# Kernel optimization log

Measured on AMD Instinct MI355X. Metric: run time of the kernel, lower is better.

The kernel has to match this reference:

```python
import jax, jax.numpy as jnp
import numpy as np

NODES = 163842
IN_FEATS = 32
OUT_FEATS = 64

def setup_inputs() -> dict:
    key = jax.random.key(0)
    k1, k2, k3, k4, k5 = jax.random.split(key, 5)
    x = jax.random.normal(k1, (NODES, IN_FEATS), dtype=jnp.float32)
    # 0-based neighbor indices (original stores 1-based and subtracts 1)
    neigh_indices = jax.random.randint(k2, (NODES, 25, 3), 0, NODES, dtype=jnp.int32)
    # barycentric interpolation weights per (node, 25 template positions, 3 triangle verts)
    neigh_weights = jax.random.uniform(k3, (NODES, 25, 3), dtype=jnp.float32)
    W = jax.random.normal(k4, (OUT_FEATS, 25 * IN_FEATS), dtype=jnp.float32) * 0.02
    b = jax.random.normal(k5, (OUT_FEATS,), dtype=jnp.float32) * 0.02
    return {"x": x, "neigh_indices": neigh_indices, "neigh_weights": neigh_weights, "W": W, "b": b}

def reference(x, neigh_indices, neigh_weights, W, b):
    nodes, c = x.shape
    # gather neighbor features: (nodes, 25, 3, in_feats)
    mat = x[neigh_indices.reshape(-1)].reshape(nodes, 25, 3, c)
    # barycentric weighted sum over the 3 triangle vertices -> (nodes, 25, in_feats)
    feat = jnp.sum(mat * neigh_weights[..., None], axis=2)
    # flatten the 25 template positions and project: (nodes, out_feats)
    feat = feat.reshape(nodes, 25 * c)
    return feat @ W.T + b
```

## Files before the change

### kernel.cpp

```cpp
#include <hip/hip_runtime.h>
#include <hip/hip_bf16.h>
#include <type_traits>

#define NNODES   163842
#define INF      32
#define OUTF     64
#define NPOS     25
#define KTOT     800
#define MT       64
#define NTHREADS 256

typedef float    f32x4 __attribute__((ext_vector_type(4)));
typedef _Float16 f16x8 __attribute__((ext_vector_type(8)));

__global__ void cvt_kernel(const float* __restrict__ x, const float* __restrict__ W,
                           _Float16* __restrict__ xh, _Float16* __restrict__ wh) {
    int tid = blockIdx.x * blockDim.x + threadIdx.x;
    int stride = gridDim.x * blockDim.x;
    const int nx8 = NNODES * INF / 8;
    const f32x4* x4 = (const f32x4*)x;
    f16x8* xh8 = (f16x8*)xh;
    for (int j = tid; j < nx8; j += stride) {
        f32x4 a = x4[2*j], b = x4[2*j+1];
        f16x8 o;
        #pragma unroll
        for (int k = 0; k < 4; ++k) { o[k] = (_Float16)a[k]; o[4+k] = (_Float16)b[k]; }
        xh8[j] = o;
    }
    f16x8* wh8 = (f16x8*)wh;
    for (int t = tid; t < NPOS * 4 * 64; t += stride) {
        const int l  = t & 63;
        const int nb = (t >> 6) & 3;
        const int p  = t >> 8;
        const int row = 16*nb + (l & 15);
        const int kb  = p*32 + (l >> 4)*8;
        const float* src = W + row * KTOT + kb;
        f16x8 o;
        #pragma unroll
        for (int j = 0; j < 8; ++j) o[j] = (_Float16)src[j];
        wh8[t] = o;
    }
}

__launch_bounds__(NTHREADS, 2)
__global__ void conv_mfma(const int* __restrict__ nidx, const float* __restrict__ nwt,
                          const _Float16* __restrict__ xh, const _Float16* __restrict__ wh,
                          const float* __restrict__ bias, float* __restrict__ out) {
    __shared__ int      idxs[MT * 75];
    __shared__ _Float16 wtsl[MT * 76];

    const int tid = threadIdx.x;
    const int blk = blockIdx.x;

    {
        const long gbase = (long)blk * (MT * 75);
        const long tot   = (long)NNODES * 75;
        #pragma unroll
        for (int it = 0; it < (MT * 75 + NTHREADS - 1) / NTHREADS; ++it) {
            int i = tid + it * NTHREADS;
            if (i < MT * 75) {
                long g = gbase + i;
                bool ok = g < tot;
                int n = i / 75, t = i % 75;
                idxs[i] = ok ? nidx[g] : 0;
                wtsl[n * 76 + t] = ok ? (_Float16)nwt[g] : (_Float16)0.0f;
            }
        }
    }

    const int lane = tid & 63;
    const int wave = tid >> 6;
    const int arow = lane & 15;
    const int kgrp = lane >> 4;
    const int irow = (wave * 16 + arow) * 75;
    const int wrow = (wave * 16 + arow) * 76;
    const int node0 = blk * MT + wave * 16;
    const _Float16* xg = xh + kgrp * 8;

    __syncthreads();

    f32x4 acc[4] = {{0,0,0,0},{0,0,0,0},{0,0,0,0},{0,0,0,0}};
    f16x8 gA[9], gB[9];
    f16x8 bA[12], bB[12];

    #define SB() __builtin_amdgcn_sched_barrier(0)

    auto BLD = [&](f16x8* b, int g, auto CNT) {
        constexpr int C = decltype(CNT)::value;
        #pragma unroll
        for (int q = 0; q < 4 * C; ++q) {
            const int f = g * 12 + q;
            b[q] = *(const f16x8*)(wh + (long)f * 512 + lane * 8);
        }
    };
    auto GATH = [&](f16x8* v, int g, auto CNT) {
        constexpr int C = decltype(CNT)::value;
        #pragma unroll
        for (int t = 0; t < 3 * C; ++t) {
            const int idx = idxs[irow + g * 9 + t];
            v[t] = *(const f16x8*)(xg + (long)idx * INF);
        }
    };
    auto COMP = [&](const f16x8* v, const f16x8* b, int g, auto CNT) {
        constexpr int C = decltype(CNT)::value;
        #pragma unroll
        for (int p = 0; p < C; ++p) {
            const int pos = g * 3 + p;
            const _Float16 w0 = wtsl[wrow + pos*3 + 0];
            const _Float16 w1 = wtsl[wrow + pos*3 + 1];
            const _Float16 w2 = wtsl[wrow + pos*3 + 2];
            f16x8 af = v[p*3+0] * w0 + v[p*3+1] * w1 + v[p*3+2] * w2;
            #pragma unroll
            for (int nb = 0; nb < 4; ++nb)
                acc[nb] = __builtin_amdgcn_mfma_f32_16x16x32_f16(b[p*4+nb], af, acc[nb], 0, 0, 0);
        }
    };

    constexpr std::integral_constant<int,3> C3{};
    constexpr std::integral_constant<int,1> C1{};

    BLD(bA,0,C3); GATH(gA,0,C3); SB();
    BLD(bB,1,C3); GATH(gB,1,C3); SB();
    COMP(gA,bA,0,C3); SB(); BLD(bA,2,C3); GATH(gA,2,C3); SB();
    COMP(gB,bB,1,C3); SB(); BLD(bB,3,C3); GATH(gB,3,C3); SB();
    COMP(gA,bA,2,C3); SB(); BLD(bA,4,C3); GATH(gA,4,C3); SB();
    COMP(gB,bB,3,C3); SB(); BLD(bB,5,C3); GATH(gB,5,C3); SB();
    COMP(gA,bA,4,C3); SB(); BLD(bA,6,C3); GATH(gA,6,C3); SB();
    COMP(gB,bB,5,C3); SB(); BLD(bB,7,C3); GATH(gB,7,C3); SB();
    COMP(gA,bA,6,C3); SB(); BLD(bA,8,C1); GATH(gA,8,C1); SB();
    COMP(gB,bB,7,C3); SB();
    COMP(gA,bA,8,C1);

    const int node = node0 + arow;
    if (node < NNODES) {
        #pragma unroll
        for (int nb = 0; nb < 4; ++nb) {
            const int cb = 16*nb + 4*kgrp;
            const f32x4 b4 = *(const f32x4*)(bias + cb);
            f32x4 o;
            #pragma unroll
            for (int r = 0; r < 4; ++r) o[r] = acc[nb][r] + b4[r];
            *(f32x4*)(out + (long)node * OUTF + cb) = o;
        }
    }
    #undef SB
}

__global__ void conv_fallback(const float* __restrict__ x, const int* __restrict__ nidx,
                              const float* __restrict__ nwt, const float* __restrict__ W,
                              const float* __restrict__ bias, float* __restrict__ out) {
    __shared__ float feat[KTOT];
    const int n = blockIdx.x;
    const int t = threadIdx.x;
    for (int e = t; e < KTOT; e += 64) {
        const int p = e >> 5, c = e & 31;
        const int ib = n * 75 + p * 3;
        float a = 0.0f;
        #pragma unroll
        for (int v = 0; v < 3; ++v)
            a += nwt[ib+v] * x[nidx[ib+v] * INF + c];
        feat[e] = a;
    }
    __syncthreads();
    float a = bias[t];
    const float* wr = W + t * KTOT;
    for (int k = 0; k < KTOT; ++k) a += feat[k] * wr[k];
    out[(long)n * OUTF + t] = a;
}

extern "C" void kernel_launch(void* const* d_in, const int* in_sizes, int n_in,
                              void* d_out, int out_size, void* d_ws, size_t ws_size,
                              hipStream_t stream) {
    const float* x    = (const float*)d_in[0];
    const int*   nidx = (const int*)  d_in[1];
    const float* nwt  = (const float*)d_in[2];
    const float* W    = (const float*)d_in[3];
    const float* bias = (const float*)d_in[4];
    float* out = (float*)d_out;

    const size_t need = (size_t)NNODES * INF * 2 + (size_t)NPOS * 4 * 64 * 8 * 2;
    if (ws_size < need) {
        conv_fallback<<<NNODES, 64, 0, stream>>>(x, nidx, nwt, W, bias, out);
        return;
    }

    _Float16* xh = (_Float16*)d_ws;
    _Float16* wh = xh + (size_t)NNODES * INF;

    cvt_kernel<<<1024, NTHREADS, 0, stream>>>(x, W, xh, wh);
    const int nblocks = (NNODES + MT - 1) / MT;
    conv_mfma<<<nblocks, NTHREADS, 0, stream>>>(nidx, nwt, xh, wh, bias, out);
}
```

Measured before the change: 179.3 us.

## Gather neighbor features directly into LDS with a per-position 3-deep load pipeline

Replaces the register-based double-buffered gather of feature rows and weight fragments with global_load_lds direct-to-LDS loads for neighbor features, plus inline-asm weight loads into a 4-slot register ring. Each template position is processed as one step with an explicit vmcnt wait, keeping three positions of loads in flight. The aim is to cut VGPR pressure and raise occupancy and memory-level parallelism for the random gathers. In exchange it adds 48KB of LDS per block, which may limit blocks per CU, and relies on hand-counted vmcnt values that must match the number of issued loads.

```diff
diff --git a/kernel.cpp b/kernel.cpp
--- a/kernel.cpp
+++ b/kernel.cpp
@@ -12,6 +12,20 @@
 
 typedef float    f32x4 __attribute__((ext_vector_type(4)));
 typedef _Float16 f16x8 __attribute__((ext_vector_type(8)));
+
+template<int N> using IC = std::integral_constant<int, N>;
+
+typedef const __attribute__((address_space(1))) void GV;
+typedef __attribute__((address_space(3))) void LV;
+
+template<int N>
+__device__ __forceinline__ void waitv_sb() {
+    static_assert(N == 0 || N == 7 || N == 14, "bad vmcnt");
+    if constexpr (N == 14)      asm volatile("s_waitcnt vmcnt(14)" ::: "memory");
+    else if constexpr (N == 7)  asm volatile("s_waitcnt vmcnt(7)"  ::: "memory");
+    else                        asm volatile("s_waitcnt vmcnt(0)"  ::: "memory");
+    __builtin_amdgcn_sched_barrier(0);
+}
 
 __global__ void cvt_kernel(const float* __restrict__ x, const float* __restrict__ W,
                            _Float16* __restrict__ xh, _Float16* __restrict__ wh) {
@@ -48,6 +62,7 @@
                           const float* __restrict__ bias, float* __restrict__ out) {
     __shared__ int      idxs[MT * 75];
     __shared__ _Float16 wtsl[MT * 76];
+    __shared__ __align__(16) _Float16 feat[4][4][3][512];
 
     const int tid = threadIdx.x;
     const int blk = blockIdx.x;
@@ -75,61 +90,60 @@
     const int irow = (wave * 16 + arow) * 75;
     const int wrow = (wave * 16 + arow) * 76;
     const int node0 = blk * MT + wave * 16;
-    const _Float16* xg = xh + kgrp * 8;
+    const _Float16* xg  = xh + kgrp * 8;
+    const char*     whl = (const char*)wh + (size_t)lane * 16;
 
     __syncthreads();
 
     f32x4 acc[4] = {{0,0,0,0},{0,0,0,0},{0,0,0,0},{0,0,0,0}};
-    f16x8 gA[9], gB[9];
-    f16x8 bA[12], bB[12];
-
-    #define SB() __builtin_amdgcn_sched_barrier(0)
-
-    auto BLD = [&](f16x8* b, int g, auto CNT) {
-        constexpr int C = decltype(CNT)::value;
-        #pragma unroll
-        for (int q = 0; q < 4 * C; ++q) {
-            const int f = g * 12 + q;
-            b[q] = *(const f16x8*)(wh + (long)f * 512 + lane * 8);
+    f16x8 bw[4][4];
+
+    auto ISSUE = [&](auto pc) {
+        constexpr int p = decltype(pc)::value;
+        constexpr int s = p & 3;
+        #pragma unroll
+        for (int v = 0; v < 3; ++v) {
+            const int idx = idxs[irow + p * 3 + v];
+            const _Float16* src = xg + (long)idx * INF;
+            __builtin_amdgcn_global_load_lds((GV*)src, (LV*)(&feat[wave][s][v][0]), 16, 0, 0);
         }
+        const char* a = whl + p * 4096;
+        asm volatile(
+            "global_load_dwordx4 %0, %4, off\n\t"
+            "global_load_dwordx4 %1, %4, off offset:1024\n\t"
+            "global_load_dwordx4 %2, %4, off offset:2048\n\t"
+            "global_load_dwordx4 %3, %4, off offset:3072"
+            : "=&v"(bw[s][0]), "=&v"(bw[s][1]), "=&v"(bw[s][2]), "=&v"(bw[s][3])
+            : "v"(a)
+            : "memory");
+        __builtin_amdgcn_sched_barrier(0);
     };
-    auto GATH = [&](f16x8* v, int g, auto CNT) {
-        constexpr int C = decltype(CNT)::value;
-        #pragma unroll
-        for (int t = 0; t < 3 * C; ++t) {
-            const int idx = idxs[irow + g * 9 + t];
-            v[t] = *(const f16x8*)(xg + (long)idx * INF);
-        }
+
+    auto STEP = [&](auto pc) {
+        constexpr int p = decltype(pc)::value;
+        waitv_sb<(p <= 22) ? 14 : ((p == 23) ? 7 : 0)>();
+        constexpr int s = p & 3;
+        const f16x8 v0 = *(const f16x8*)&feat[wave][s][0][lane * 8];
+        const f16x8 v1 = *(const f16x8*)&feat[wave][s][1][lane * 8];
+        const f16x8 v2 = *(const f16x8*)&feat[wave][s][2][lane * 8];
+        const _Float16 w0 = wtsl[wrow + p * 3 + 0];
+        const _Float16 w1 = wtsl[wrow + p * 3 + 1];
+        const _Float16 w2 = wtsl[wrow + p * 3 + 2];
+        const f16x8 af = v0 * w0 + v1 * w1 + v2 * w2;
+        #pragma unroll
+        for (int nb = 0; nb < 4; ++nb)
+            acc[nb] = __builtin_amdgcn_mfma_f32_16x16x32_f16(bw[s][nb], af, acc[nb], 0, 0, 0);
+        __builtin_amdgcn_sched_barrier(0);
+        if constexpr (p + 3 < NPOS) ISSUE(IC<p + 3>{});
     };
-    auto COMP = [&](const f16x8* v, const f16x8* b, int g, auto CNT) {
-        constexpr int C = decltype(CNT)::value;
-        #pragma unroll
-        for (int p = 0; p < C; ++p) {
-            const int pos = g * 3 + p;
-            const _Float16 w0 = wtsl[wrow + pos*3 + 0];
-            const _Float16 w1 = wtsl[wrow + pos*3 + 1];
-            const _Float16 w2 = wtsl[wrow + pos*3 + 2];
-            f16x8 af = v[p*3+0] * w0 + v[p*3+1] * w1 + v[p*3+2] * w2;
-            #pragma unroll
-            for (int nb = 0; nb < 4; ++nb)
-                acc[nb] = __builtin_amdgcn_mfma_f32_16x16x32_f16(b[p*4+nb], af, acc[nb], 0, 0, 0);
-        }
-    };
-
-    constexpr std::integral_constant<int,3> C3{};
-    constexpr std::integral_constant<int,1> C1{};
-
-    BLD(bA,0,C3); GATH(gA,0,C3); SB();
-    BLD(bB,1,C3); GATH(gB,1,C3); SB();
-    COMP(gA,bA,0,C3); SB(); BLD(bA,2,C3); GATH(gA,2,C3); SB();
-    COMP(gB,bB,1,C3); SB(); BLD(bB,3,C3); GATH(gB,3,C3); SB();
-    COMP(gA,bA,2,C3); SB(); BLD(bA,4,C3); GATH(gA,4,C3); SB();
-    COMP(gB,bB,3,C3); SB(); BLD(bB,5,C3); GATH(gB,5,C3); SB();
-    COMP(gA,bA,4,C3); SB(); BLD(bA,6,C3); GATH(gA,6,C3); SB();
-    COMP(gB,bB,5,C3); SB(); BLD(bB,7,C3); GATH(gB,7,C3); SB();
-    COMP(gA,bA,6,C3); SB(); BLD(bA,8,C1); GATH(gA,8,C1); SB();
-    COMP(gB,bB,7,C3); SB();
-    COMP(gA,bA,8,C1);
+
+    ISSUE(IC<0>{}); ISSUE(IC<1>{}); ISSUE(IC<2>{});
+
+    STEP(IC<0>{});  STEP(IC<1>{});  STEP(IC<2>{});  STEP(IC<3>{});  STEP(IC<4>{});
+    STEP(IC<5>{});  STEP(IC<6>{});  STEP(IC<7>{});  STEP(IC<8>{});  STEP(IC<9>{});
+    STEP(IC<10>{}); STEP(IC<11>{}); STEP(IC<12>{}); STEP(IC<13>{}); STEP(IC<14>{});
+    STEP(IC<15>{}); STEP(IC<16>{}); STEP(IC<17>{}); STEP(IC<18>{}); STEP(IC<19>{});
+    STEP(IC<20>{}); STEP(IC<21>{}); STEP(IC<22>{}); STEP(IC<23>{}); STEP(IC<24>{});
 
     const int node = node0 + arow;
     if (node < NNODES) {
@@ -143,7 +157,6 @@
             *(f32x4*)(out + (long)node * OUTF + cb) = o;
         }
     }
-    #undef SB
 }
 
 __global__ void conv_fallback(const float* __restrict__ x, const int* __restrict__ nidx,
```

After: 178.7 us (median of 2 runs). About the same (-0.4%).

## Stage W in LDS via async loads and use a 4-deep gather pipeline

Applied to the files above, without the earlier changes.

The whole pre-converted fp16 weight matrix is copied into shared memory with global_load_lds, so per-step B fragments come from LDS rather than repeated global loads. The neighbour gather becomes a rolling 4-stage prefetch written in inline asm, with explicit vmcnt waits before each MFMA step. The block grows to 128 nodes and 8 waves. In exchange it uses about 100KB of LDS per block, which limits occupancy, and relies on hand-counted waitcnt values being correct.

```diff
diff --git a/kernel.cpp b/kernel.cpp
--- a/kernel.cpp
+++ b/kernel.cpp
@@ -1,17 +1,20 @@
 #include <hip/hip_runtime.h>
 #include <hip/hip_bf16.h>
-#include <type_traits>
 
 #define NNODES   163842
 #define INF      32
 #define OUTF     64
 #define NPOS     25
 #define KTOT     800
-#define MT       64
-#define NTHREADS 256
+#define MT       128
+#define NTHREADS 512
+#define NWAVES   8
 
 typedef float    f32x4 __attribute__((ext_vector_type(4)));
 typedef _Float16 f16x8 __attribute__((ext_vector_type(8)));
+
+typedef const __attribute__((address_space(1))) void GV;
+typedef __attribute__((address_space(3))) void LV;
 
 __global__ void cvt_kernel(const float* __restrict__ x, const float* __restrict__ W,
                            _Float16* __restrict__ xh, _Float16* __restrict__ wh) {
@@ -46,90 +49,92 @@
 __global__ void conv_mfma(const int* __restrict__ nidx, const float* __restrict__ nwt,
                           const _Float16* __restrict__ xh, const _Float16* __restrict__ wh,
                           const float* __restrict__ bias, float* __restrict__ out) {
+    __shared__ __align__(16) _Float16 whl[NPOS * 4 * 64 * 8];
     __shared__ int      idxs[MT * 75];
-    __shared__ _Float16 wtsl[MT * 76];
+    __shared__ _Float16 wtsl[MT * 75];
 
-    const int tid = threadIdx.x;
-    const int blk = blockIdx.x;
+    const int tid  = threadIdx.x;
+    const int blk  = blockIdx.x;
+    const int lane = tid & 63;
+    const int wave = tid >> 6;
 
+    for (int i = wave; i < NPOS * 4; i += NWAVES) {
+        __builtin_amdgcn_global_load_lds((GV*)((const char*)wh + i * 1024 + lane * 16),
+                                         (LV*)((char*)whl + i * 1024), 16, 0, 0);
+    }
     {
         const long gbase = (long)blk * (MT * 75);
         const long tot   = (long)NNODES * 75;
-        #pragma unroll
-        for (int it = 0; it < (MT * 75 + NTHREADS - 1) / NTHREADS; ++it) {
-            int i = tid + it * NTHREADS;
-            if (i < MT * 75) {
-                long g = gbase + i;
-                bool ok = g < tot;
-                int n = i / 75, t = i % 75;
-                idxs[i] = ok ? nidx[g] : 0;
-                wtsl[n * 76 + t] = ok ? (_Float16)nwt[g] : (_Float16)0.0f;
-            }
+        for (int i = tid; i < MT * 75; i += NTHREADS) {
+            long g = gbase + i;
+            bool ok = g < tot;
+            idxs[i] = ok ? nidx[g] : 0;
+            wtsl[i] = ok ? (_Float16)nwt[g] : (_Float16)0.0f;
         }
     }
 
-    const int lane = tid & 63;
-    const int wave = tid >> 6;
-    const int arow = lane & 15;
-    const int kgrp = lane >> 4;
-    const int irow = (wave * 16 + arow) * 75;
-    const int wrow = (wave * 16 + arow) * 76;
+    const int arow  = lane & 15;
+    const int kgrp  = lane >> 4;
+    const int irow  = (wave * 16 + arow) * 75;
     const int node0 = blk * MT + wave * 16;
     const _Float16* xg = xh + kgrp * 8;
 
     __syncthreads();
 
-    f32x4 acc[4] = {{0,0,0,0},{0,0,0,0},{0,0,0,0},{0,0,0,0}};
-    f16x8 gA[9], gB[9];
-    f16x8 bA[12], bB[12];
+    f32x4 acc0 = {0,0,0,0}, acc1 = {0,0,0,0}, acc2 = {0,0,0,0}, acc3 = {0,0,0,0};
+    f16x8 g00, g01, g02, g10, g11, g12, g20, g21, g22, g30, g31, g32;
 
-    #define SB() __builtin_amdgcn_sched_barrier(0)
+#define ISSUE(P, S) do {                                                        \
+        const int _p = (P);                                                     \
+        const int _i0 = idxs[irow + _p*3 + 0];                                  \
+        const int _i1 = idxs[irow + _p*3 + 1];                                  \
+        const int _i2 = idxs[irow + _p*3 + 2];                                  \
+        const _Float16* _a0 = xg + (long)_i0 * INF;                             \
+        const _Float16* _a1 = xg + (long)_i1 * INF;                             \
+        const _Float16* _a2 = xg + (long)_i2 * INF;                             \
+        asm volatile("global_load_dwordx4 %0, %1, off" : "=&v"(g##S##0) : "v"(_a0)); \
+        asm volatile("global_load_dwordx4 %0, %1, off" : "=&v"(g##S##1) : "v"(_a1)); \
+        asm volatile("global_load_dwordx4 %0, %1, off" : "=&v"(g##S##2) : "v"(_a2)); \
+    } while (0)
 
-    auto BLD = [&](f16x8* b, int g, auto CNT) {
-        constexpr int C = decltype(CNT)::value;
-        #pragma unroll
-        for (int q = 0; q < 4 * C; ++q) {
-            const int f = g * 12 + q;
-            b[q] = *(const f16x8*)(wh + (long)f * 512 + lane * 8);
-        }
-    };
-    auto GATH = [&](f16x8* v, int g, auto CNT) {
-        constexpr int C = decltype(CNT)::value;
-        #pragma unroll
-        for (int t = 0; t < 3 * C; ++t) {
-            const int idx = idxs[irow + g * 9 + t];
-            v[t] = *(const f16x8*)(xg + (long)idx * INF);
-        }
-    };
-    auto COMP = [&](const f16x8* v, const f16x8* b, int g, auto CNT) {
-        constexpr int C = decltype(CNT)::value;
-        #pragma unroll
-        for (int p = 0; p < C; ++p) {
-            const int pos = g * 3 + p;
-            const _Float16 w0 = wtsl[wrow + pos*3 + 0];
-            const _Float16 w1 = wtsl[wrow + pos*3 + 1];
-            const _Float16 w2 = wtsl[wrow + pos*3 + 2];
-            f16x8 af = v[p*3+0] * w0 + v[p*3+1] * w1 + v[p*3+2] * w2;
-            #pragma unroll
-            for (int nb = 0; nb < 4; ++nb)
-                acc[nb] = __builtin_amdgcn_mfma_f32_16x16x32_f16(b[p*4+nb], af, acc[nb], 0, 0, 0);
-        }
-    };
+#define STEP(P, S, VM, PI) do {                                                 \
+        const int _p = (P);                                                     \
+        const f16x8* _bwp = (const f16x8*)whl + _p * 256 + lane;                \
+        const f16x8 _b0 = _bwp[0];                                              \
+        const f16x8 _b1 = _bwp[64];                                             \
+        const f16x8 _b2 = _bwp[128];                                            \
+        const f16x8 _b3 = _bwp[192];                                            \
+        const _Float16 _w0 = wtsl[irow + _p*3 + 0];                             \
+        const _Float16 _w1 = wtsl[irow + _p*3 + 1];                             \
+        const _Float16 _w2 = wtsl[irow + _p*3 + 2];                             \
+        asm volatile("s_waitcnt vmcnt(" #VM ")" ::: "memory");                  \
+        __builtin_amdgcn_sched_barrier(0);                                      \
+        const f16x8 _af = g##S##0 * _w0 + g##S##1 * _w1 + g##S##2 * _w2;        \
+        acc0 = __builtin_amdgcn_mfma_f32_16x16x32_f16(_b0, _af, acc0, 0, 0, 0); \
+        acc1 = __builtin_amdgcn_mfma_f32_16x16x32_f16(_b1, _af, acc1, 0, 0, 0); \
+        acc2 = __builtin_amdgcn_mfma_f32_16x16x32_f16(_b2, _af, acc2, 0, 0, 0); \
+        acc3 = __builtin_amdgcn_mfma_f32_16x16x32_f16(_b3, _af, acc3, 0, 0, 0); \
+        __builtin_amdgcn_sched_barrier(0);                                      \
+        if ((PI) >= 0) ISSUE((PI), S);                                          \
+        __builtin_amdgcn_sched_barrier(0);                                      \
+    } while (0)
 
-    constexpr std::integral_constant<int,3> C3{};
-    constexpr std::integral_constant<int,1> C1{};
+    ISSUE(0, 0); ISSUE(1, 1); ISSUE(2, 2); ISSUE(3, 3);
 
-    BLD(bA,0,C3); GATH(gA,0,C3); SB();
-    BLD(bB,1,C3); GATH(gB,1,C3); SB();
-    COMP(gA,bA,0,C3); SB(); BLD(bA,2,C3); GATH(gA,2,C3); SB();
-    COMP(gB,bB,1,C3); SB(); BLD(bB,3,C3); GATH(gB,3,C3); SB();
-    COMP(gA,bA,2,C3); SB(); BLD(bA,4,C3); GATH(gA,4,C3); SB();
-    COMP(gB,bB,3,C3); SB(); BLD(bB,5,C3); GATH(gB,5,C3); SB();
-    COMP(gA,bA,4,C3); SB(); BLD(bA,6,C3); GATH(gA,6,C3); SB();
-    COMP(gB,bB,5,C3); SB(); BLD(bB,7,C3); GATH(gB,7,C3); SB();
-    COMP(gA,bA,6,C3); SB(); BLD(bA,8,C1); GATH(gA,8,C1); SB();
-    COMP(gB,bB,7,C3); SB();
-    COMP(gA,bA,8,C1);
+    for (int pp = 0; pp < 20; pp += 4) {
+        STEP(pp + 0, 0, 9, pp + 4);
+        STEP(pp + 1, 1, 9, pp + 5);
+        STEP(pp + 2, 2, 9, pp + 6);
+        STEP(pp + 3, 3, 9, pp + 7);
+    }
+    STEP(20, 0, 9, 24);
+    STEP(21, 1, 9, -1);
+    STEP(22, 2, 6, -1);
+    STEP(23, 3, 3, -1);
+    STEP(24, 0, 0, -1);
+
+#undef ISSUE
+#undef STEP
 
     const int node = node0 + arow;
     if (node < NNODES) {
@@ -139,11 +144,10 @@
             const f32x4 b4 = *(const f32x4*)(bias + cb);
             f32x4 o;
             #pragma unroll
-            for (int r = 0; r < 4; ++r) o[r] = acc[nb][r] + b4[r];
+            for (int r = 0; r < 4; ++r) o[r] = (nb == 0 ? acc0 : nb == 1 ? acc1 : nb == 2 ? acc2 : acc3)[r] + b4[r];
             *(f32x4*)(out + (long)node * OUTF + cb) = o;
         }
     }
-    #undef SB
 }
 
 __global__ void conv_fallback(const float* __restrict__ x, const int* __restrict__ nidx,
@@ -187,7 +191,7 @@
     _Float16* xh = (_Float16*)d_ws;
     _Float16* wh = xh + (size_t)NNODES * INF;
 
-    cvt_kernel<<<1024, NTHREADS, 0, stream>>>(x, W, xh, wh);
+    cvt_kernel<<<1024, 256, 0, stream>>>(x, W, xh, wh);
     const int nblocks = (NNODES + MT - 1) / MT;
     conv_mfma<<<nblocks, NTHREADS, 0, stream>>>(nidx, nwt, xh, wh, bias, out);
 }
```

Result: slower. 187.9 us (+4.8%).
